# Optimization experiments

Hardware: AMD Instinct MI355X
Metric: run time of the kernel (lower is better)

Reference implementation:

```python
import jax, jax.numpy as jnp
import numpy as np
from jax import lax

B, S, HDIM = 4, 2048, 1024
H, D, L = 16, 64, 128
NB = S // L
EPS = 1e-8


def setup_inputs() -> dict:
    key = jax.random.key(0)
    ks = jax.random.split(key, 16)
    std = 0.02
    inp = {
        'f_in': jax.random.normal(ks[0], (B, S, HDIM), jnp.float32),
        'i_in': jax.random.normal(ks[1], (B, S, HDIM), jnp.float32),
        'z_in': jax.random.normal(ks[2], (B, S, HDIM), jnp.float32),
        'o_in': jax.random.normal(ks[3], (B, S, HDIM), jnp.float32),
        'c0': jax.random.normal(ks[4], (B, H, D), jnp.float32),
        'h0': jax.random.normal(ks[5], (B, H, D), jnp.float32),
        # weights stored (in, out) so forward is x @ W + b
        'Wf': std * jax.random.normal(ks[6], (HDIM, H * D), jnp.float32),
        'bf': jnp.zeros((H * D,), jnp.float32),
        'Wi': std * jax.random.normal(ks[7], (HDIM, H * D), jnp.float32),
        'bi': jnp.zeros((H * D,), jnp.float32),
        'Wz': std * jax.random.normal(ks[8], (HDIM, H * D), jnp.float32),
        'bz': jnp.zeros((H * D,), jnp.float32),
        'Wo': std * jax.random.normal(ks[9], (HDIM, H * D), jnp.float32),
        'bo': jnp.zeros((H * D,), jnp.float32),
        'Wp': std * jax.random.normal(ks[10], (H * D, HDIM), jnp.float32),
        'bp': jnp.zeros((HDIM,), jnp.float32),
    }
    return inp


def _to_blocks(x):
    # (B,S,H*D) -> (NB, B, H, D, L), matching torch view+permute(1,0,3,4,2)
    return jnp.transpose(x.reshape(B, NB, L, H, D), (1, 0, 3, 4, 2))


def _qlstm(f_in, i_in, z_in, o_in, c0, Wf, bf, Wi, bi, Wz, bz, Wo, bo, Wp, bp):
    fx = _to_blocks(f_in @ Wf + bf)
    ix = _to_blocks(i_in @ Wi + bi)
    zx = _to_blocks(z_in @ Wz + bz)
    ox = _to_blocks(o_in @ Wo + bo)

    f = jax.nn.sigmoid(fx + 1.0)              # (NB,B,H,D,L)
    o = jax.nn.sigmoid(ox)
    update = jax.nn.sigmoid(ix) * jnp.tanh(zx)

    kk = jnp.arange(L)[:, None]
    ll = jnp.arange(L + 1)[None, :]
    ones_mask = ll >= kk + 1                   # (L, L+1): filled with 1.0
    zeros_mask = ll >= kk + 2                  # (L, L+1): zeroed out

    def block_step(c, blk):
        fb, ob, ub = blk                       # each (B,H,D,L)
        cf = jnp.concatenate([fb, jnp.ones(fb.shape[:-1] + (1,), fb.dtype)], axis=-1)  # (B,H,D,L+1)
        Fm = jnp.broadcast_to(cf[..., None, :], fb.shape[:-1] + (L, L + 1))
        Fm = jnp.where(ones_mask, 1.0, Fm)
        # reversed log-cumsum-exp along last axis (decay products)
        Fm = jnp.exp(jnp.flip(jnp.cumsum(jnp.flip(jnp.log(Fm + EPS), -1), -1), -1)) - EPS
        Fm = jnp.where(zeros_mask, 0.0, Fm)    # (B,H,D,L,L+1)
        u = jnp.concatenate([c[..., None], ub], axis=-1)   # (B,H,D,L+1)
        cs = jnp.einsum('bhdkl,bhdl->bhdk', Fm, u)          # (B,H,D,L)
        hs = ob * jnp.tanh(cs)
        return cs[..., -1], hs

    last_c, hs = lax.scan(block_step, c0, (f, o, update))   # hs: (NB,B,H,D,L)
    last_h = hs[-1, ..., -1]
    y = jnp.transpose(hs, (1, 0, 4, 2, 3)).reshape(B, S, H * D)
    y = y @ Wp + bp                            # (B,S,HDIM)
    return y, last_c, last_h


def reference(f_in, i_in, z_in, o_in, c0, h0, Wf, bf, Wi, bi, Wz, bz, Wo, bo, Wp, bp):
    y, last_c, last_h = _qlstm(f_in, i_in, z_in, o_in, c0,
                               Wf, bf, Wi, bi, Wz, bz, Wo, bo, Wp, bp)
    return y, last_c, last_h
```

## Files before the change

### kernel.cpp

```cpp
#include <hip/hip_runtime.h>
#include <hip/hip_bf16.h>
#include <stdint.h>

constexpr int GM = 8192;
constexpr int GK = 1024;
constexpr int GN = 1024;
constexpr size_t NACT = (size_t)GM * GN;
constexpr int CHUNK = 32;
constexpr int NCHUNK = 64;
constexpr int NCH = 4096;
constexpr int NT = GK / 64;

#define DEVINL __device__ __forceinline__

typedef __attribute__((ext_vector_type(8))) short bf16x8;
typedef __attribute__((ext_vector_type(4))) float f32x4;

DEVINL float sigmoidf_(float x) { return 1.0f / (1.0f + __expf(-x)); }

DEVINL unsigned short f2bf(float x) {
  unsigned int u = __builtin_bit_cast(unsigned int, x);
  unsigned int rnd = 0x7fffu + ((u >> 16) & 1u);
  return (unsigned short)((u + rnd) >> 16);
}
DEVINL float bf2f(unsigned short u) {
  unsigned int x = ((unsigned int)u) << 16;
  return __builtin_bit_cast(float, x);
}

DEVINL void gload16(const void* g, void* l) {
  __builtin_amdgcn_global_load_lds(
      (const __attribute__((address_space(1))) unsigned int*)g,
      (__attribute__((address_space(3))) unsigned int*)l, 16, 0, 0);
}

__global__ void cvt4_kernel(const float* __restrict__ s0, const float* __restrict__ s1,
                            const float* __restrict__ s2, const float* __restrict__ s3,
                            unsigned short* __restrict__ d0, unsigned short* __restrict__ d1,
                            unsigned short* __restrict__ d2, unsigned short* __restrict__ d3,
                            int n4) {
  const float* s;
  unsigned short* d;
  switch (blockIdx.y) {
    case 0: s = s0; d = d0; break;
    case 1: s = s1; d = d1; break;
    case 2: s = s2; d = d2; break;
    default: s = s3; d = d3; break;
  }
  int stride = gridDim.x * blockDim.x;
  for (int i = blockIdx.x * blockDim.x + threadIdx.x; i < n4; i += stride) {
    float4 v = ((const float4*)s)[i];
    ushort4 o;
    o.x = f2bf(v.x); o.y = f2bf(v.y); o.z = f2bf(v.z); o.w = f2bf(v.w);
    ((ushort4*)d)[i] = o;
  }
}

struct TPtrs {
  const float* src[5];
  unsigned short* dst[5];
};

__global__ void transpose_cvt_all(TPtrs p) {
  const float* __restrict__ W = p.src[blockIdx.z];
  unsigned short* __restrict__ Wt = p.dst[blockIdx.z];
  __shared__ float tile[32][33];
  int n0 = blockIdx.x * 32, k0 = blockIdx.y * 32;
  int tx = threadIdx.x & 31, ty = threadIdx.x >> 5;
#pragma unroll
  for (int i = 0; i < 32; i += 8)
    tile[ty + i][tx] = W[(size_t)(k0 + ty + i) * GN + n0 + tx];
  __syncthreads();
#pragma unroll
  for (int i = 0; i < 32; i += 8)
    Wt[(size_t)(n0 + ty + i) * GK + k0 + tx] = f2bf(tile[tx][ty + i]);
}

DEVINL void gemm256_core(const unsigned short* __restrict__ A,
                         const unsigned short* __restrict__ W,
                         char* lds, int tid, int wave, int lane,
                         int bm, int bn, f32x4 (&acc)[8][4]) {
  const int Ah = wave >> 2;
  const int wn = (wave & 3) * 64;
  const int lrow = lane & 15;
  const int lgrp = lane >> 4;

  const char* gsrc[8];
  char* ldst[8];
  {
    const char* Ag = (const char*)A;
    const char* Wg = (const char*)W;
#pragma unroll
    for (int hh = 0; hh < 4; ++hh)
#pragma unroll
      for (int j = 0; j < 2; ++j) {
        const int lbyte = j * 8192 + tid * 16;
        const int row = lbyte >> 7;
        const int gcb = (lbyte & 127) ^ ((row & 7) << 4);
        const int i = hh * 2 + j;
        gsrc[i] = (hh < 2)
            ? Ag + (size_t)(bm * 256 + hh * 128 + row) * 2048 + gcb
            : Wg + (size_t)(bn * 256 + (hh - 2) * 128 + row) * 2048 + gcb;
        ldst[i] = lds + (hh >= 2 ? 32768 : 0) + (hh & 1) * 16384 + j * 8192 +
                  wave * 1024;
      }
  }

#pragma unroll
  for (int i = 0; i < 8; ++i) gload16(gsrc[i], ldst[i]);

  bf16x8 aF[4][2], bF[4][2];

  for (int t = 0; t < NT; ++t) {
    const int cur = t & 1;
    const int obuf = (cur ^ 1) * 65536;
    const char* Abase = lds + cur * 65536 + Ah * 16384;
    const char* Bbase = lds + cur * 65536 + 32768;
    const int nk = (t + 1 < NT) ? (t + 1) : (NT - 1);
    const size_t koff = (size_t)nk * 128;

#pragma unroll
    for (int i = 0; i < 4; ++i) gload16(gsrc[i] + koff, ldst[i] + obuf);
    asm volatile("s_waitcnt vmcnt(4)" ::: "memory");
    __builtin_amdgcn_s_barrier();
    __builtin_amdgcn_sched_barrier(0);
#pragma unroll
    for (int m = 0; m < 4; ++m)
#pragma unroll
      for (int ks = 0; ks < 2; ++ks) {
        const int r = m * 16 + lrow;
        const int cb = ks * 64 + lgrp * 16;
        aF[m][ks] = *(const bf16x8*)(Abase + r * 128 + (cb ^ ((r & 7) << 4)));
      }
#pragma unroll
    for (int n = 0; n < 2; ++n)
#pragma unroll
      for (int ks = 0; ks < 2; ++ks) {
        const int nr = wn + n * 16 + lrow;
        const int cb = ks * 64 + lgrp * 16;
        bF[n][ks] = *(const bf16x8*)(Bbase + nr * 128 + (cb ^ ((nr & 7) << 4)));
      }
    __builtin_amdgcn_s_setprio(1);
#pragma unroll
    for (int m = 0; m < 4; ++m)
#pragma unroll
      for (int n = 0; n < 2; ++n)
#pragma unroll
        for (int ks = 0; ks < 2; ++ks)
          acc[m][n] = __builtin_amdgcn_mfma_f32_16x16x32_bf16(aF[m][ks], bF[n][ks],
                                                              acc[m][n], 0, 0, 0);
    __builtin_amdgcn_s_setprio(0);

#pragma unroll
    for (int n = 2; n < 4; ++n)
#pragma unroll
      for (int ks = 0; ks < 2; ++ks) {
        const int nr = wn + n * 16 + lrow;
        const int cb = ks * 64 + lgrp * 16;
        bF[n][ks] = *(const bf16x8*)(Bbase + nr * 128 + (cb ^ ((nr & 7) << 4)));
      }
#pragma unroll
    for (int i = 4; i < 8; ++i) gload16(gsrc[i] + koff, ldst[i] + obuf);
    __builtin_amdgcn_s_barrier();
    asm volatile("s_waitcnt lgkmcnt(0)" ::: "memory");
    __builtin_amdgcn_sched_barrier(0);
    __builtin_amdgcn_s_setprio(1);
#pragma unroll
    for (int m = 0; m < 4; ++m)
#pragma unroll
      for (int n = 2; n < 4; ++n)
#pragma unroll
        for (int ks = 0; ks < 2; ++ks)
          acc[m][n] = __builtin_amdgcn_mfma_f32_16x16x32_bf16(aF[m][ks], bF[n][ks],
                                                              acc[m][n], 0, 0, 0);
    __builtin_amdgcn_s_setprio(0);

#pragma unroll
    for (int m = 0; m < 4; ++m)
#pragma unroll
      for (int ks = 0; ks < 2; ++ks) {
        const int r = (m + 4) * 16 + lrow;
        const int cb = ks * 64 + lgrp * 16;
        aF[m][ks] = *(const bf16x8*)(Abase + r * 128 + (cb ^ ((r & 7) << 4)));
      }
    __builtin_amdgcn_s_barrier();
    asm volatile("s_waitcnt lgkmcnt(0)" ::: "memory");
    __builtin_amdgcn_sched_barrier(0);
    __builtin_amdgcn_s_setprio(1);
#pragma unroll
    for (int m = 0; m < 4; ++m)
#pragma unroll
      for (int n = 2; n < 4; ++n)
#pragma unroll
        for (int ks = 0; ks < 2; ++ks)
          acc[m + 4][n] = __builtin_amdgcn_mfma_f32_16x16x32_bf16(aF[m][ks], bF[n][ks],
                                                                  acc[m + 4][n], 0, 0, 0);
    __builtin_amdgcn_s_setprio(0);

    __builtin_amdgcn_s_barrier();
    __builtin_amdgcn_s_setprio(1);
#pragma unroll
    for (int m = 0; m < 4; ++m)
#pragma unroll
      for (int n = 0; n < 2; ++n)
#pragma unroll
        for (int ks = 0; ks < 2; ++ks)
          acc[m + 4][n] = __builtin_amdgcn_mfma_f32_16x16x32_bf16(aF[m][ks], bF[n][ks],
                                                                  acc[m + 4][n], 0, 0, 0);
    __builtin_amdgcn_s_setprio(0);
  }
}

struct GateArgs {
  const unsigned short* A[4];
  const unsigned short* W[4];
  const float* bias[4];
  unsigned short* out[4];
};

__global__ __launch_bounds__(512, 2) void gemm_gates8(GateArgs ga) {
  extern __shared__ char lds[];
  const int tid = threadIdx.x;
  const int wave = tid >> 6, lane = tid & 63;
  const int bm = blockIdx.x, bn = blockIdx.y, gz = blockIdx.z;
  const int wm = (wave >> 2) * 128, wn = (wave & 3) * 64;
  const int lrow = lane & 15, lgrp = lane >> 4;

  f32x4 acc[8][4];
#pragma unroll
  for (int m = 0; m < 8; ++m)
#pragma unroll
    for (int n = 0; n < 4; ++n) acc[m][n] = (f32x4){0.f, 0.f, 0.f, 0.f};

  gemm256_core(ga.A[gz], ga.W[gz], lds, tid, wave, lane, bm, bn, acc);

  const float* bias = ga.bias[gz];
  unsigned short* out = ga.out[gz];
  float bv[4];
#pragma unroll
  for (int n = 0; n < 4; ++n) bv[n] = bias[bn * 256 + wn + n * 16 + lrow];

#pragma unroll
  for (int m = 0; m < 8; ++m)
#pragma unroll
    for (int n = 0; n < 4; ++n) {
      const int gc = bn * 256 + wn + n * 16 + lrow;
#pragma unroll
      for (int j = 0; j < 4; ++j) {
        const int gr = bm * 256 + wm + m * 16 + lgrp * 4 + j;
        float v = acc[m][n][j] + bv[n];
        if (gz == 0) v = sigmoidf_(v + 1.0f);
        else if (gz == 1) v = sigmoidf_(v);
        out[(size_t)gr * GN + gc] = f2bf(v);
      }
    }
}

__global__ __launch_bounds__(512, 2) void gemm_proj8(
    const unsigned short* __restrict__ A, const unsigned short* __restrict__ W,
    const float* __restrict__ bias, float* __restrict__ out) {
  extern __shared__ char lds[];
  const int tid = threadIdx.x;
  const int wave = tid >> 6, lane = tid & 63;
  const int bm = blockIdx.x, bn = blockIdx.y;
  const int wm = (wave >> 2) * 128, wn = (wave & 3) * 64;
  const int lrow = lane & 15, lgrp = lane >> 4;

  f32x4 acc[8][4];
#pragma unroll
  for (int m = 0; m < 8; ++m)
#pragma unroll
    for (int n = 0; n < 4; ++n) acc[m][n] = (f32x4){0.f, 0.f, 0.f, 0.f};

  gemm256_core(A, W, lds, tid, wave, lane, bm, bn, acc);

  float bv[4];
#pragma unroll
  for (int n = 0; n < 4; ++n) bv[n] = bias[bn * 256 + wn + n * 16 + lrow];

#pragma unroll
  for (int m = 0; m < 8; ++m)
#pragma unroll
    for (int n = 0; n < 4; ++n) {
      const int gc = bn * 256 + wn + n * 16 + lrow;
#pragma unroll
      for (int j = 0; j < 4; ++j) {
        const int gr = bm * 256 + wm + m * 16 + lgrp * 4 + j;
        out[(size_t)gr * GN + gc] = acc[m][n][j] + bv[n];
      }
    }
}

__global__ void scan_phaseA_kernel(const unsigned short* __restrict__ F,
                                   const unsigned short* __restrict__ Ip,
                                   const unsigned short* __restrict__ Zp,
                                   float* __restrict__ Pt, float* __restrict__ Ct) {
  int tid = blockIdx.x * blockDim.x + threadIdx.x;
  int ch = tid & (NCH - 1), chunk = tid >> 12;
  int b = ch >> 10, n = ch & 1023;
  size_t base = ((size_t)(b * 2048 + chunk * CHUNK)) * 1024 + n;
  float c = 0.f, P = 1.f;
#pragma unroll 8
  for (int t = 0; t < CHUNK; ++t) {
    size_t idx = base + (size_t)t * 1024;
    float f = bf2f(F[idx]);
    float u = sigmoidf_(bf2f(Ip[idx])) * tanhf(bf2f(Zp[idx]));
    c = __builtin_fmaf(f, c, u);
    P *= f;
  }
  Pt[tid] = P;
  Ct[tid] = c;
}

__global__ void scan_combine_kernel(const float* __restrict__ Pt,
                                    const float* __restrict__ Ct,
                                    const float* __restrict__ c0,
                                    float* __restrict__ Cin,
                                    float* __restrict__ last_c) {
  int ch = blockIdx.x * blockDim.x + threadIdx.x;
  float c = c0[ch];
#pragma unroll
  for (int j = 0; j < NCHUNK; ++j) {
    Cin[j * NCH + ch] = c;
    c = __builtin_fmaf(Pt[j * NCH + ch], c, Ct[j * NCH + ch]);
  }
  last_c[ch] = c;
}

__global__ void scan_phaseC_kernel(const unsigned short* __restrict__ F,
                                   const unsigned short* __restrict__ Ip,
                                   const unsigned short* __restrict__ Zp,
                                   const unsigned short* __restrict__ O,
                                   const float* __restrict__ Cin,
                                   unsigned short* __restrict__ Hb,
                                   float* __restrict__ last_h) {
  int tid = blockIdx.x * blockDim.x + threadIdx.x;
  int ch = tid & (NCH - 1), chunk = tid >> 12;
  int b = ch >> 10, n = ch & 1023;
  size_t base = ((size_t)(b * 2048 + chunk * CHUNK)) * 1024 + n;
  float c = Cin[tid];
  float h = 0.f;
#pragma unroll 8
  for (int t = 0; t < CHUNK; ++t) {
    size_t idx = base + (size_t)t * 1024;
    float f = bf2f(F[idx]);
    float u = sigmoidf_(bf2f(Ip[idx])) * tanhf(bf2f(Zp[idx]));
    float o = bf2f(O[idx]);
    c = __builtin_fmaf(f, c, u);
    h = o * tanhf(c);
    Hb[idx] = f2bf(h);
  }
  if (chunk == NCHUNK - 1) last_h[ch] = h;
}

extern "C" void kernel_launch(void* const* d_in, const int* in_sizes, int n_in,
                              void* d_out, int out_size, void* d_ws, size_t ws_size,
                              hipStream_t stream) {
  const float* f_in = (const float*)d_in[0];
  const float* i_in = (const float*)d_in[1];
  const float* z_in = (const float*)d_in[2];
  const float* o_in = (const float*)d_in[3];
  const float* c0 = (const float*)d_in[4];
  const float* Wf = (const float*)d_in[6];
  const float* bf_ = (const float*)d_in[7];
  const float* Wi = (const float*)d_in[8];
  const float* bi = (const float*)d_in[9];
  const float* Wz = (const float*)d_in[10];
  const float* bz = (const float*)d_in[11];
  const float* Wo = (const float*)d_in[12];
  const float* bo = (const float*)d_in[13];
  const float* Wp = (const float*)d_in[14];
  const float* bp = (const float*)d_in[15];

  float* y = (float*)d_out;
  float* last_c = y + NACT;
  float* last_h = last_c + NCH;

  char* w = (char*)d_ws;
  const size_t ABYTES = NACT * 2;
  const size_t WBYTES = (size_t)GK * GN * 2;
  unsigned short* Af = (unsigned short*)(w + 0 * ABYTES);
  unsigned short* Ai = (unsigned short*)(w + 1 * ABYTES);
  unsigned short* Az = (unsigned short*)(w + 2 * ABYTES);
  unsigned short* Ao = (unsigned short*)(w + 3 * ABYTES);
  char* wt = w + 4 * ABYTES;
  unsigned short* Wtf = (unsigned short*)(wt + 0 * WBYTES);
  unsigned short* Wti = (unsigned short*)(wt + 1 * WBYTES);
  unsigned short* Wtz = (unsigned short*)(wt + 2 * WBYTES);
  unsigned short* Wto = (unsigned short*)(wt + 3 * WBYTES);
  unsigned short* Wtp = (unsigned short*)(wt + 4 * WBYTES);
  char* gp = wt + 5 * WBYTES;
  unsigned short* F = (unsigned short*)(gp + 0 * ABYTES);
  unsigned short* O = (unsigned short*)(gp + 1 * ABYTES);
  unsigned short* Ip = (unsigned short*)(gp + 2 * ABYTES);
  unsigned short* Zp = (unsigned short*)(gp + 3 * ABYTES);
  unsigned short* Hb = Af;
  char* sp = gp + 4 * ABYTES;
  const size_t SBYTES = (size_t)NCH * NCHUNK * 4;
  float* Pt = (float*)(sp + 0 * SBYTES);
  float* Ct = (float*)(sp + 1 * SBYTES);
  float* Cin = (float*)(sp + 2 * SBYTES);

  (void)hipFuncSetAttribute((const void*)gemm_gates8,
                            hipFuncAttributeMaxDynamicSharedMemorySize, 131072);
  (void)hipFuncSetAttribute((const void*)gemm_proj8,
                            hipFuncAttributeMaxDynamicSharedMemorySize, 131072);

  cvt4_kernel<<<dim3(1024, 4), 256, 0, stream>>>(
      f_in, o_in, i_in, z_in, Af, Ao, Ai, Az, (int)(NACT / 4));

  TPtrs tp;
  tp.src[0] = Wf; tp.src[1] = Wi; tp.src[2] = Wz; tp.src[3] = Wo; tp.src[4] = Wp;
  tp.dst[0] = Wtf; tp.dst[1] = Wti; tp.dst[2] = Wtz; tp.dst[3] = Wto; tp.dst[4] = Wtp;
  transpose_cvt_all<<<dim3(32, 32, 5), 256, 0, stream>>>(tp);

  GateArgs ga;
  ga.A[0] = Af;  ga.A[1] = Ao;  ga.A[2] = Ai;  ga.A[3] = Az;
  ga.W[0] = Wtf; ga.W[1] = Wto; ga.W[2] = Wti; ga.W[3] = Wtz;
  ga.bias[0] = bf_; ga.bias[1] = bo; ga.bias[2] = bi; ga.bias[3] = bz;
  ga.out[0] = F; ga.out[1] = O; ga.out[2] = Ip; ga.out[3] = Zp;
  gemm_gates8<<<dim3(GM / 256, GN / 256, 4), 512, 131072, stream>>>(ga);

  scan_phaseA_kernel<<<(NCH * NCHUNK) / 256, 256, 0, stream>>>(F, Ip, Zp, Pt, Ct);
  scan_combine_kernel<<<NCH / 256, 256, 0, stream>>>(Pt, Ct, c0, Cin, last_c);
  scan_phaseC_kernel<<<(NCH * NCHUNK) / 256, 256, 0, stream>>>(F, Ip, Zp, O, Cin, Hb,
                                                               last_h);

  gemm_proj8<<<dim3(GM / 256, GN / 256), 512, 131072, stream>>>(Hb, Wtp, bp, y);
}
```

Measured before the change: 206.1 us.

## Fuse prep kernels, precompute gate activations, retile projection GEMM to 256x128

Merges the activation bf16 conversion and the weight transpose into a single prep launch. Moves the sigmoid/tanh for the i and z gates into the gate GEMM epilogue, so both scan phases only multiply stored values instead of recomputing the transcendentals twice. Replaces the projection GEMM with a 256x128-tile variant that uses smaller LDS and launches twice as many blocks, to improve occupancy and wave balance. Also removes one barrier from the shared GEMM core, which could risk an LDS race if that barrier was protecting buffer reuse.

Result: slower. 213.6 us (+3.6%).

```diff
diff --git a/kernel.cpp b/kernel.cpp
--- a/kernel.cpp
+++ b/kernel.cpp
@@ -34,46 +34,45 @@
       (__attribute__((address_space(3))) unsigned int*)l, 16, 0, 0);
 }
 
-__global__ void cvt4_kernel(const float* __restrict__ s0, const float* __restrict__ s1,
-                            const float* __restrict__ s2, const float* __restrict__ s3,
-                            unsigned short* __restrict__ d0, unsigned short* __restrict__ d1,
-                            unsigned short* __restrict__ d2, unsigned short* __restrict__ d3,
-                            int n4) {
-  const float* s;
-  unsigned short* d;
-  switch (blockIdx.y) {
-    case 0: s = s0; d = d0; break;
-    case 1: s = s1; d = d1; break;
-    case 2: s = s2; d = d2; break;
-    default: s = s3; d = d3; break;
-  }
-  int stride = gridDim.x * blockDim.x;
-  for (int i = blockIdx.x * blockDim.x + threadIdx.x; i < n4; i += stride) {
-    float4 v = ((const float4*)s)[i];
-    ushort4 o;
-    o.x = f2bf(v.x); o.y = f2bf(v.y); o.z = f2bf(v.z); o.w = f2bf(v.w);
-    ((ushort4*)d)[i] = o;
-  }
-}
-
-struct TPtrs {
-  const float* src[5];
-  unsigned short* dst[5];
+#define SB() __builtin_amdgcn_sched_barrier(0)
+
+struct PrepArgs {
+  const float* csrc[4];
+  unsigned short* cdst[4];
+  const float* tsrc[5];
+  unsigned short* tdst[5];
 };
 
-__global__ void transpose_cvt_all(TPtrs p) {
-  const float* __restrict__ W = p.src[blockIdx.z];
-  unsigned short* __restrict__ Wt = p.dst[blockIdx.z];
-  __shared__ float tile[32][33];
-  int n0 = blockIdx.x * 32, k0 = blockIdx.y * 32;
-  int tx = threadIdx.x & 31, ty = threadIdx.x >> 5;
-#pragma unroll
-  for (int i = 0; i < 32; i += 8)
-    tile[ty + i][tx] = W[(size_t)(k0 + ty + i) * GN + n0 + tx];
-  __syncthreads();
-#pragma unroll
-  for (int i = 0; i < 32; i += 8)
-    Wt[(size_t)(n0 + ty + i) * GK + k0 + tx] = f2bf(tile[tx][ty + i]);
+__global__ __launch_bounds__(256) void prep_kernel(PrepArgs p) {
+  const int bx = blockIdx.x;
+  if (bx < 4096) {
+    const float* s = p.csrc[bx >> 10];
+    unsigned short* d = p.cdst[bx >> 10];
+    int i = (bx & 1023) * 256 + threadIdx.x;
+    const int stride = 1024 * 256;
+#pragma unroll
+    for (int it = 0; it < 8; ++it, i += stride) {
+      float4 v = ((const float4*)s)[i];
+      ushort4 o;
+      o.x = f2bf(v.x); o.y = f2bf(v.y); o.z = f2bf(v.z); o.w = f2bf(v.w);
+      ((ushort4*)d)[i] = o;
+    }
+  } else {
+    const int t = bx - 4096;
+    const float* __restrict__ W = p.tsrc[t >> 10];
+    unsigned short* __restrict__ Wt = p.tdst[t >> 10];
+    const int rem = t & 1023;
+    const int n0 = (rem & 31) * 32, k0 = (rem >> 5) * 32;
+    __shared__ float tile[32][33];
+    int tx = threadIdx.x & 31, ty = threadIdx.x >> 5;
+#pragma unroll
+    for (int i = 0; i < 32; i += 8)
+      tile[ty + i][tx] = W[(size_t)(k0 + ty + i) * GN + n0 + tx];
+    __syncthreads();
+#pragma unroll
+    for (int i = 0; i < 32; i += 8)
+      Wt[(size_t)(n0 + ty + i) * GK + k0 + tx] = f2bf(tile[tx][ty + i]);
+  }
 }
 
 DEVINL void gemm256_core(const unsigned short* __restrict__ A,
@@ -123,7 +122,7 @@
     for (int i = 0; i < 4; ++i) gload16(gsrc[i] + koff, ldst[i] + obuf);
     asm volatile("s_waitcnt vmcnt(4)" ::: "memory");
     __builtin_amdgcn_s_barrier();
-    __builtin_amdgcn_sched_barrier(0);
+    SB();
 #pragma unroll
     for (int m = 0; m < 4; ++m)
 #pragma unroll
@@ -163,7 +162,7 @@
     for (int i = 4; i < 8; ++i) gload16(gsrc[i] + koff, ldst[i] + obuf);
     __builtin_amdgcn_s_barrier();
     asm volatile("s_waitcnt lgkmcnt(0)" ::: "memory");
-    __builtin_amdgcn_sched_barrier(0);
+    SB();
     __builtin_amdgcn_s_setprio(1);
 #pragma unroll
     for (int m = 0; m < 4; ++m)
@@ -185,7 +184,7 @@
       }
     __builtin_amdgcn_s_barrier();
     asm volatile("s_waitcnt lgkmcnt(0)" ::: "memory");
-    __builtin_amdgcn_sched_barrier(0);
+    SB();
     __builtin_amdgcn_s_setprio(1);
 #pragma unroll
     for (int m = 0; m < 4; ++m)
@@ -197,7 +196,6 @@
                                                                   acc[m + 4][n], 0, 0, 0);
     __builtin_amdgcn_s_setprio(0);
 
-    __builtin_amdgcn_s_barrier();
     __builtin_amdgcn_s_setprio(1);
 #pragma unroll
     for (int m = 0; m < 4; ++m)
@@ -250,39 +248,132 @@
         const int gr = bm * 256 + wm + m * 16 + lgrp * 4 + j;
         float v = acc[m][n][j] + bv[n];
         if (gz == 0) v = sigmoidf_(v + 1.0f);
-        else if (gz == 1) v = sigmoidf_(v);
+        else if (gz == 3) v = tanhf(v);
+        else v = sigmoidf_(v);
         out[(size_t)gr * GN + gc] = f2bf(v);
       }
     }
 }
 
-__global__ __launch_bounds__(512, 2) void gemm_proj8(
+__global__ __launch_bounds__(512, 2) void gemm_proj_bn128(
     const unsigned short* __restrict__ A, const unsigned short* __restrict__ W,
     const float* __restrict__ bias, float* __restrict__ out) {
   extern __shared__ char lds[];
   const int tid = threadIdx.x;
   const int wave = tid >> 6, lane = tid & 63;
   const int bm = blockIdx.x, bn = blockIdx.y;
-  const int wm = (wave >> 2) * 128, wn = (wave & 3) * 64;
+  const int wm = (wave >> 2) * 128, wn = (wave & 3) * 32;
   const int lrow = lane & 15, lgrp = lane >> 4;
 
-  f32x4 acc[8][4];
+  f32x4 acc[8][2];
 #pragma unroll
   for (int m = 0; m < 8; ++m)
 #pragma unroll
-    for (int n = 0; n < 4; ++n) acc[m][n] = (f32x4){0.f, 0.f, 0.f, 0.f};
-
-  gemm256_core(A, W, lds, tid, wave, lane, bm, bn, acc);
-
-  float bv[4];
-#pragma unroll
-  for (int n = 0; n < 4; ++n) bv[n] = bias[bn * 256 + wn + n * 16 + lrow];
+    for (int n = 0; n < 2; ++n) acc[m][n] = (f32x4){0.f, 0.f, 0.f, 0.f};
+
+  const char* gsrc[6];
+  char* ldst[6];
+  {
+    const char* Ag = (const char*)A;
+    const char* Wg = (const char*)W;
+#pragma unroll
+    for (int i = 0; i < 4; ++i) {
+      const int lbyte = i * 8192 + tid * 16;
+      const int row = lbyte >> 7;
+      const int gcb = (lbyte & 127) ^ ((row & 7) << 4);
+      gsrc[i] = Ag + (size_t)(bm * 256 + row) * 2048 + gcb;
+      ldst[i] = lds + i * 8192 + wave * 1024;
+    }
+#pragma unroll
+    for (int j = 0; j < 2; ++j) {
+      const int lbyte = j * 8192 + tid * 16;
+      const int row = lbyte >> 7;
+      const int gcb = (lbyte & 127) ^ ((row & 7) << 4);
+      gsrc[4 + j] = Wg + (size_t)(bn * 128 + row) * 2048 + gcb;
+      ldst[4 + j] = lds + 65536 + j * 8192 + wave * 1024;
+    }
+  }
+
+#pragma unroll
+  for (int i = 0; i < 6; ++i) gload16(gsrc[i], ldst[i]);
+
+  bf16x8 aLo[4][2], aHi[4][2], bF[2][2];
+
+  for (int t = 0; t < NT; ++t) {
+    const int cur = t & 1;
+    const int obufA = (cur ^ 1) * 32768;
+    const int obufB = (cur ^ 1) * 16384;
+    const char* Abase = lds + cur * 32768;
+    const char* Bbase = lds + 65536 + cur * 16384;
+    const int nk = (t + 1 < NT) ? (t + 1) : (NT - 1);
+    const size_t koff = (size_t)nk * 128;
+
+#pragma unroll
+    for (int i = 0; i < 4; ++i) gload16(gsrc[i] + koff, ldst[i] + obufA);
+    asm volatile("s_waitcnt vmcnt(4)" ::: "memory");
+    __builtin_amdgcn_s_barrier();
+    SB();
+#pragma unroll
+    for (int m = 0; m < 4; ++m)
+#pragma unroll
+      for (int ks = 0; ks < 2; ++ks) {
+        const int r = wm + m * 16 + lrow;
+        const int cb = ks * 64 + lgrp * 16;
+        aLo[m][ks] = *(const bf16x8*)(Abase + r * 128 + (cb ^ ((r & 7) << 4)));
+      }
+#pragma unroll
+    for (int n = 0; n < 2; ++n)
+#pragma unroll
+      for (int ks = 0; ks < 2; ++ks) {
+        const int nr = wn + n * 16 + lrow;
+        const int cb = ks * 64 + lgrp * 16;
+        bF[n][ks] = *(const bf16x8*)(Bbase + nr * 128 + (cb ^ ((nr & 7) << 4)));
+      }
+    __builtin_amdgcn_s_setprio(1);
+#pragma unroll
+    for (int m = 0; m < 4; ++m)
+#pragma unroll
+      for (int n = 0; n < 2; ++n)
+#pragma unroll
+        for (int ks = 0; ks < 2; ++ks)
+          acc[m][n] = __builtin_amdgcn_mfma_f32_16x16x32_bf16(aLo[m][ks], bF[n][ks],
+                                                              acc[m][n], 0, 0, 0);
+    __builtin_amdgcn_s_setprio(0);
+
+#pragma unroll
+    for (int m = 0; m < 4; ++m)
+#pragma unroll
+      for (int ks = 0; ks < 2; ++ks) {
+        const int r = wm + (m + 4) * 16 + lrow;
+        const int cb = ks * 64 + lgrp * 16;
+        aHi[m][ks] = *(const bf16x8*)(Abase + r * 128 + (cb ^ ((r & 7) << 4)));
+      }
+#pragma unroll
+    for (int j = 4; j < 6; ++j) gload16(gsrc[j] + koff, ldst[j] + obufB);
+    __builtin_amdgcn_s_barrier();
+    asm volatile("s_waitcnt lgkmcnt(0)" ::: "memory");
+    SB();
+    __builtin_amdgcn_s_setprio(1);
+#pragma unroll
+    for (int m = 0; m < 4; ++m)
+#pragma unroll
+      for (int n = 0; n < 2; ++n)
+#pragma unroll
+        for (int ks = 0; ks < 2; ++ks)
+          acc[m + 4][n] = __builtin_amdgcn_mfma_f32_16x16x32_bf16(aHi[m][ks], bF[n][ks],
+                                                                  acc[m + 4][n], 0, 0, 0);
+    __builtin_amdgcn_s_setprio(0);
+  }
+
+  float bv[2];
+#pragma unroll
+  for (int n = 0; n < 2; ++n) bv[n] = bias[bn * 128 + wn + n * 16 + lrow];
 
 #pragma unroll
   for (int m = 0; m < 8; ++m)
 #pragma unroll
-    for (int n = 0; n < 4; ++n) {
-      const int gc = bn * 256 + wn + n * 16 + lrow;
+    for (int n = 0; n < 2; ++n) {
+      const int gc = bn * 128 + wn + n * 16 + lrow;
 #pragma unroll
       for (int j = 0; j < 4; ++j) {
         const int gr = bm * 256 + wm + m * 16 + lgrp * 4 + j;
@@ -292,8 +383,8 @@
 }
 
 __global__ void scan_phaseA_kernel(const unsigned short* __restrict__ F,
-                                   const unsigned short* __restrict__ Ip,
-                                   const unsigned short* __restrict__ Zp,
+                                   const unsigned short* __restrict__ Si,
+                                   const unsigned short* __restrict__ Tz,
                                    float* __restrict__ Pt, float* __restrict__ Ct) {
   int tid = blockIdx.x * blockDim.x + threadIdx.x;
   int ch = tid & (NCH - 1), chunk = tid >> 12;
@@ -304,7 +395,7 @@
   for (int t = 0; t < CHUNK; ++t) {
     size_t idx = base + (size_t)t * 1024;
     float f = bf2f(F[idx]);
-    float u = sigmoidf_(bf2f(Ip[idx])) * tanhf(bf2f(Zp[idx]));
+    float u = bf2f(Si[idx]) * bf2f(Tz[idx]);
     c = __builtin_fmaf(f, c, u);
     P *= f;
   }
@@ -328,8 +419,8 @@
 }
 
 __global__ void scan_phaseC_kernel(const unsigned short* __restrict__ F,
-                                   const unsigned short* __restrict__ Ip,
-                                   const unsigned short* __restrict__ Zp,
+                                   const unsigned short* __restrict__ Si,
+                                   const unsigned short* __restrict__ Tz,
                                    const unsigned short* __restrict__ O,
                                    const float* __restrict__ Cin,
                                    unsigned short* __restrict__ Hb,
@@ -344,7 +435,7 @@
   for (int t = 0; t < CHUNK; ++t) {
     size_t idx = base + (size_t)t * 1024;
     float f = bf2f(F[idx]);
-    float u = sigmoidf_(bf2f(Ip[idx])) * tanhf(bf2f(Zp[idx]));
+    float u = bf2f(Si[idx]) * bf2f(Tz[idx]);
     float o = bf2f(O[idx]);
     c = __builtin_fmaf(f, c, u);
     h = o * tanhf(c);
@@ -392,8 +483,8 @@
   char* gp = wt + 5 * WBYTES;
   unsigned short* F = (unsigned short*)(gp + 0 * ABYTES);
   unsigned short* O = (unsigned short*)(gp + 1 * ABYTES);
-  unsigned short* Ip = (unsigned short*)(gp + 2 * ABYTES);
-  unsigned short* Zp = (unsigned short*)(gp + 3 * ABYTES);
+  unsigned short* Si = (unsigned short*)(gp + 2 * ABYTES);
+  unsigned short* Tz = (unsigned short*)(gp + 3 * ABYTES);
   unsigned short* Hb = Af;
   char* sp = gp + 4 * ABYTES;
   const size_t SBYTES = (size_t)NCH * NCHUNK * 4;
@@ -403,28 +494,27 @@
 
   (void)hipFuncSetAttribute((const void*)gemm_gates8,
                             hipFuncAttributeMaxDynamicSharedMemorySize, 131072);
-  (void)hipFuncSetAttribute((const void*)gemm_proj8,
-                            hipFuncAttributeMaxDynamicSharedMemorySize, 131072);
-
-  cvt4_kernel<<<dim3(1024, 4), 256, 0, stream>>>(
-      f_in, o_in, i_in, z_in, Af, Ao, Ai, Az, (int)(NACT / 4));
-
-  TPtrs tp;
-  tp.src[0] = Wf; tp.src[1] = Wi; tp.src[2] = Wz; tp.src[3] = Wo; tp.src[4] = Wp;
-  tp.dst[0] = Wtf; tp.dst[1] = Wti; tp.dst[2] = Wtz; tp.dst[3] = Wto; tp.dst[4] = Wtp;
-  transpose_cvt_all<<<dim3(32, 32, 5), 256, 0, stream>>>(tp);
+  (void)hipFuncSetAttribute((const void*)gemm_proj_bn128,
+                            hipFuncAttributeMaxDynamicSharedMemorySize, 98304);
+
+  PrepArgs pa;
+  pa.csrc[0] = f_in; pa.csrc[1] = o_in; pa.csrc[2] = i_in; pa.csrc[3] = z_in;
+  pa.cdst[0] = Af;   pa.cdst[1] = Ao;   pa.cdst[2] = Ai;   pa.cdst[3] = Az;
+  pa.tsrc[0] = Wf; pa.tsrc[1] = Wi; pa.tsrc[2] = Wz; pa.tsrc[3] = Wo; pa.tsrc[4] = Wp;
+  pa.tdst[0] = Wtf; pa.tdst[1] = Wti; pa.tdst[2] = Wtz; pa.tdst[3] = Wto; pa.tdst[4] = Wtp;
+  prep_kernel<<<9216, 256, 0, stream>>>(pa);
 
   GateArgs ga;
   ga.A[0] = Af;  ga.A[1] = Ao;  ga.A[2] = Ai;  ga.A[3] = Az;
   ga.W[0] = Wtf; ga.W[1] = Wto; ga.W[2] = Wti; ga.W[3] = Wtz;
   ga.bias[0] = bf_; ga.bias[1] = bo; ga.bias[2] = bi; ga.bias[3] = bz;
-  ga.out[0] = F; ga.out[1] = O; ga.out[2] = Ip; ga.out[3] = Zp;
+  ga.out[0] = F; ga.out[1] = O; ga.out[2] = Si; ga.out[3] = Tz;
   gemm_gates8<<<dim3(GM / 256, GN / 256, 4), 512, 131072, stream>>>(ga);
 
-  scan_phaseA_kernel<<<(NCH * NCHUNK) / 256, 256, 0, stream>>>(F, Ip, Zp, Pt, Ct);
+  scan_phaseA_kernel<<<(NCH * NCHUNK) / 256, 256, 0, stream>>>(F, Si, Tz, Pt, Ct);
   scan_combine_kernel<<<NCH / 256, 256, 0, stream>>>(Pt, Ct, c0, Cin, last_c);
-  scan_phaseC_kernel<<<(NCH * NCHUNK) / 256, 256, 0, stream>>>(F, Ip, Zp, O, Cin, Hb,
+  scan_phaseC_kernel<<<(NCH * NCHUNK) / 256, 256, 0, stream>>>(F, Si, Tz, O, Cin, Hb,
                                                                last_h);
 
-  gemm_proj8<<<dim3(GM / 256, GN / 256), 512, 131072, stream>>>(Hb, Wtp, bp, y);
-}
+  gemm_proj_bn128<<<dim3(GM / 256, GN / 128), 512, 98304, stream>>>(Hb, Wtp, bp, y);
+}
```
